# Performance work log

Measured on AMD Instinct MI355X. Metric: run time of the kernel, lower is better.

The kernel has to match this reference:

```python
import jax, jax.numpy as jnp
import numpy as np

# --- configuration (mirrors init_kwargs) ---
N_G = (256, 256, 128, 128)   # tem.hyper['n_g'] per-module sizes
N_ACTIONS = 4                 # tem action space
NUM_STATES = 4096
BATCH = 16384
G_TOTAL = sum(N_G)            # 768


def setup_inputs() -> dict:
    key = jax.random.key(0)
    ks = jax.random.split(key, 4 + len(N_G))
    inp = {
        "current_state_index": jax.random.randint(ks[0], (BATCH,), 0, NUM_STATES),
        "action_index": jax.random.randint(ks[1], (BATCH,), 0, N_ACTIONS),
        # xavier-ish init scale for embedding / classifier
        "emb": jax.random.normal(ks[2], (NUM_STATES, G_TOTAL), jnp.float32) * 0.02,
        "W_cls": jax.random.normal(ks[3], (NUM_STATES, G_TOTAL), jnp.float32) * 0.02,
        "b_cls": jnp.zeros((NUM_STATES,), jnp.float32),
    }
    # per-module bank of action-conditioned transition matrices D_a: [n_actions, n_g_f, n_g_f]
    for f, n in enumerate(N_G):
        inp[f"D{f}"] = jax.random.normal(ks[4 + f], (N_ACTIONS, n, n), jnp.float32) * (1.0 / np.sqrt(n))
    return inp


def _transition(g_f, D_f, onehot):
    # Routed action-conditioned transition (replaces the CPU per-action loop):
    # delta[b, j] = sum_i D_f[a_b, j, i] * g_f[b, i], dispatched via one-hot over actions.
    delta = jnp.einsum('aji,bi,ba->bj', D_f, g_f, onehot)
    # TEM generative clamp activation f_g_clamp
    return jnp.clip(g_f + delta, -1.0, 1.0)


def reference(current_state_index, action_index, emb, D0, D1, D2, D3, W_cls, b_cls):
    g_flat = emb[current_state_index]                                   # [B, G_TOTAL]
    onehot = jax.nn.one_hot(action_index, N_ACTIONS, dtype=g_flat.dtype)  # [B, A]
    # _split_g: slice flat grid code into TEM modules
    g_mods = jnp.split(g_flat, np.cumsum(np.array(N_G))[:-1].tolist(), axis=1)
    Ds = (D0, D1, D2, D3)
    g_next = [_transition(g_f, D_f, onehot) for g_f, D_f in zip(g_mods, Ds)]
    g_next_flat = jnp.concatenate(g_next, axis=1)                       # [B, G_TOTAL]
    logits = g_next_flat @ W_cls.T + b_cls                              # [B, NUM_STATES]
    return logits, g_next_flat
```

## Files before the change

### kernel.cpp

```cpp
#include <hip/hip_runtime.h>
#include <hip/hip_bf16.h>
#include <stdint.h>


typedef __attribute__((ext_vector_type(8))) short short8;
typedef __attribute__((ext_vector_type(4))) float floatx4;

__device__ __forceinline__ float bf2f(short s) {
    unsigned int u = ((unsigned int)(unsigned short)s) << 16;
    float f;
    __builtin_memcpy(&f, &u, 4);
    return f;
}
__device__ __forceinline__ short f2bf(float f) {
    unsigned int u;
    __builtin_memcpy(&u, &f, 4);
    u = (u + 0x7FFFu + ((u >> 16) & 1u)) >> 16;
    return (short)u;
}

#define GLLDS16(g, l)                                                                     \
    __builtin_amdgcn_global_load_lds((const __attribute__((address_space(1))) void*)(g),  \
                                     (__attribute__((address_space(3))) void*)(l), 16, 0, 0)

__global__ __launch_bounds__(256) void prep_kernel(
    const int* __restrict__ state, const float* __restrict__ emb,
    const float* __restrict__ W, const float* __restrict__ D0,
    const float* __restrict__ D1, const float* __restrict__ D2,
    const float* __restrict__ D3, short* __restrict__ A1,
    short* __restrict__ Wb, short* __restrict__ Db) {
    long e = (long)blockIdx.x * 256 + threadIdx.x;
    const float* src;
    short* dst;
    long di;
    if (e < 3145728L) {
        int b = (int)(e / 192);
        int cc = (int)(e % 192);
        int s = state[b];
        src = emb + (long)s * 768 + cc * 4;
        dst = A1; di = e;
    } else if (e < 3932160L) {
        long t = e - 3145728L;
        src = W + t * 4; dst = Wb; di = t;
    } else if (e < 3997696L) {
        long t = e - 3932160L;
        src = D0 + t * 4; dst = Db; di = t;
    } else if (e < 4063232L) {
        long t = e - 3997696L;
        src = D1 + t * 4; dst = Db + 262144; di = t;
    } else if (e < 4079616L) {
        long t = e - 4063232L;
        src = D2 + t * 4; dst = Db + 524288; di = t;
    } else {
        long t = e - 4079616L;
        src = D3 + t * 4; dst = Db + 589824; di = t;
    }
    float4 v = *(const float4*)src;
    union { ushort4 u4; short s4[4]; } o;
    o.s4[0] = f2bf(v.x); o.s4[1] = f2bf(v.y);
    o.s4[2] = f2bf(v.z); o.s4[3] = f2bf(v.w);
    *(ushort4*)(dst + di * 4) = o.u4;
}

__global__ __launch_bounds__(256) void trans_gemm_kernel(
    const short* __restrict__ A, const short* __restrict__ Bm,
    const int* __restrict__ act, float* __restrict__ gnext,
    short* __restrict__ A2, int n, int K) {
    __shared__ short Ash[128 * 64];
    __shared__ short Bsh[128 * 64];
    const int tid = threadIdx.x;
    const int lane = tid & 63;
    const int w = tid >> 6;
    const int wm = w & 1, wn = w >> 1;
    const int bn = blockIdx.x, bm = blockIdx.y;
    const long arow0 = (long)bm * 128;
    const long brow0 = (long)bn * 128;
    const int lrow = lane & 15;
    const int q = lane >> 4;

    floatx4 acc[4][4] = {};

    for (int k0 = 0; k0 < K; k0 += 64) {
        #pragma unroll
        for (int it = 0; it < 4; ++it) {
            int c = it * 256 + tid;
            int r = c >> 3, cc = c & 7;
            int gc = cc ^ (r & 7);
            GLLDS16(A + (arow0 + r) * 768 + k0 + gc * 8, &Ash[c * 8]);
            GLLDS16(Bm + (brow0 + r) * (long)n + k0 + gc * 8, &Bsh[c * 8]);
        }
        __syncthreads();
        #pragma unroll
        for (int kk = 0; kk < 2; ++kk) {
            short8 af[4], bv[4];
            #pragma unroll
            for (int mi = 0; mi < 4; ++mi) {
                int rr = wm * 64 + mi * 16 + lrow;
                int ch = (kk * 4 + q) ^ (rr & 7);
                af[mi] = *(const short8*)&Ash[rr * 64 + ch * 8];
            }
            #pragma unroll
            for (int ni = 0; ni < 4; ++ni) {
                int rr = wn * 64 + ni * 16 + lrow;
                int ch = (kk * 4 + q) ^ (rr & 7);
                bv[ni] = *(const short8*)&Bsh[rr * 64 + ch * 8];
            }
            #pragma unroll
            for (int mi = 0; mi < 4; ++mi)
                #pragma unroll
                for (int ni = 0; ni < 4; ++ni)
                    acc[mi][ni] = __builtin_amdgcn_mfma_f32_16x16x32_bf16(
                        af[mi], bv[ni], acc[mi][ni], 0, 0, 0);
        }
        __syncthreads();
    }

    const int tile_action = (bn * 128) / n;
    const int jb = bn * 128 - tile_action * n + wn * 64;
    const int rowbase = bm * 128 + wm * 64;
    #pragma unroll
    for (int mi = 0; mi < 4; ++mi) {
        #pragma unroll
        for (int r = 0; r < 4; ++r) {
            int row = rowbase + mi * 16 + q * 4 + r;
            if (act[row] == tile_action) {
                #pragma unroll
                for (int ni = 0; ni < 4; ++ni) {
                    int jl = jb + ni * 16 + lrow;
                    long idx = (long)row * 768 + jl;
                    float g = bf2f(A[idx]);
                    float v = g + acc[mi][ni][r];
                    v = fminf(1.0f, fmaxf(-1.0f, v));
                    gnext[idx] = v;
                    A2[idx] = f2bf(v);
                }
            }
        }
    }
}

__global__ __launch_bounds__(256) void cls_gemm_kernel(
    const short* __restrict__ A, const short* __restrict__ Bm,
    const float* __restrict__ bias, float* __restrict__ out) {
    __shared__ short Ash[128 * 64];
    __shared__ short Bsh[128 * 64];
    const int tid = threadIdx.x;
    const int lane = tid & 63;
    const int w = tid >> 6;
    const int wm = w & 1, wn = w >> 1;
    const int bn = blockIdx.x, bm = blockIdx.y;
    const long arow0 = (long)bm * 128;
    const long brow0 = (long)bn * 128;
    const int lrow = lane & 15;
    const int q = lane >> 4;

    floatx4 acc[4][4] = {};

    for (int k0 = 0; k0 < 768; k0 += 64) {
        #pragma unroll
        for (int it = 0; it < 4; ++it) {
            int c = it * 256 + tid;
            int r = c >> 3, cc = c & 7;
            int gc = cc ^ (r & 7);
            GLLDS16(A + (arow0 + r) * 768 + k0 + gc * 8, &Ash[c * 8]);
            GLLDS16(Bm + (brow0 + r) * 768 + k0 + gc * 8, &Bsh[c * 8]);
        }
        __syncthreads();
        #pragma unroll
        for (int kk = 0; kk < 2; ++kk) {
            short8 af[4], bv[4];
            #pragma unroll
            for (int mi = 0; mi < 4; ++mi) {
                int rr = wm * 64 + mi * 16 + lrow;
                int ch = (kk * 4 + q) ^ (rr & 7);
                af[mi] = *(const short8*)&Ash[rr * 64 + ch * 8];
            }
            #pragma unroll
            for (int ni = 0; ni < 4; ++ni) {
                int rr = wn * 64 + ni * 16 + lrow;
                int ch = (kk * 4 + q) ^ (rr & 7);
                bv[ni] = *(const short8*)&Bsh[rr * 64 + ch * 8];
            }
            #pragma unroll
            for (int mi = 0; mi < 4; ++mi)
                #pragma unroll
                for (int ni = 0; ni < 4; ++ni)
                    acc[mi][ni] = __builtin_amdgcn_mfma_f32_16x16x32_bf16(
                        af[mi], bv[ni], acc[mi][ni], 0, 0, 0);
        }
        __syncthreads();
    }

    const int rowbase = bm * 128 + wm * 64;
    const int colbase = bn * 128 + wn * 64;
    #pragma unroll
    for (int mi = 0; mi < 4; ++mi) {
        #pragma unroll
        for (int r = 0; r < 4; ++r) {
            int row = rowbase + mi * 16 + q * 4 + r;
            #pragma unroll
            for (int ni = 0; ni < 4; ++ni) {
                int col = colbase + ni * 16 + lrow;
                out[(long)row * 4096 + col] = acc[mi][ni][r] + bias[col];
            }
        }
    }
}

extern "C" void kernel_launch(void* const* d_in, const int* in_sizes, int n_in,
                              void* d_out, int out_size, void* d_ws, size_t ws_size,
                              hipStream_t stream) {
    const int* state  = (const int*)d_in[0];
    const int* act    = (const int*)d_in[1];
    const float* emb  = (const float*)d_in[2];
    const float* W    = (const float*)d_in[3];
    const float* bias = (const float*)d_in[4];
    const float* D0   = (const float*)d_in[5];
    const float* D1   = (const float*)d_in[6];
    const float* D2   = (const float*)d_in[7];
    const float* D3   = (const float*)d_in[8];

    float* logits = (float*)d_out;
    float* gnext  = logits + 67108864L;

    short* A1 = (short*)d_ws;
    short* A2 = A1 + 12582912L;
    short* Wb = A2 + 12582912L;
    short* Db = Wb + 3145728L;

    prep_kernel<<<16000, 256, 0, stream>>>(state, emb, W, D0, D1, D2, D3, A1, Wb, Db);

    trans_gemm_kernel<<<dim3(8, 128), 256, 0, stream>>>(A1, Db, act, gnext, A2, 256, 256);
    trans_gemm_kernel<<<dim3(8, 128), 256, 0, stream>>>(A1 + 256, Db + 262144, act,
                                                        gnext + 256, A2 + 256, 256, 256);
    trans_gemm_kernel<<<dim3(4, 128), 256, 0, stream>>>(A1 + 512, Db + 524288, act,
                                                        gnext + 512, A2 + 512, 128, 128);
    trans_gemm_kernel<<<dim3(4, 128), 256, 0, stream>>>(A1 + 640, Db + 589824, act,
                                                        gnext + 640, A2 + 640, 128, 128);

    cls_gemm_kernel<<<dim3(32, 128), 256, 0, stream>>>(A2, Wb, bias, logits);
}
```

Before: 541.0 us.

## Sort batch rows by action so transition GEMM computes only the matching action

```diff
diff --git a/kernel.cpp b/kernel.cpp
--- a/kernel.cpp
+++ b/kernel.cpp
@@ -23,12 +23,72 @@
     __builtin_amdgcn_global_load_lds((const __attribute__((address_space(1))) void*)(g),  \
                                      (__attribute__((address_space(3))) void*)(l), 16, 0, 0)
 
+#define ROWS_PAD 16896
+
+__global__ __launch_bounds__(1024) void setup_kernel(const int* __restrict__ act,
+                                                     int* __restrict__ meta,
+                                                     int* __restrict__ s2o) {
+    const int tid = threadIdx.x;
+    const int lane = tid & 63;
+    const int w = tid >> 6;
+    __shared__ int lc[16][4];
+    int c0 = 0, c1 = 0, c2 = 0, c3 = 0;
+    for (int i = tid; i < 16384; i += 1024) {
+        int a = act[i];
+        unsigned long long m0 = __ballot(a == 0);
+        unsigned long long m1 = __ballot(a == 1);
+        unsigned long long m2 = __ballot(a == 2);
+        unsigned long long m3 = __ballot(a == 3);
+        if (lane == 0) {
+            c0 += __popcll(m0); c1 += __popcll(m1);
+            c2 += __popcll(m2); c3 += __popcll(m3);
+        }
+    }
+    if (lane == 0) { lc[w][0] = c0; lc[w][1] = c1; lc[w][2] = c2; lc[w][3] = c3; }
+    for (int i = tid; i < ROWS_PAD; i += 1024) s2o[i] = -1;
+    __syncthreads();
+    if (tid == 0) {
+        int base = 0;
+        for (int k = 0; k < 4; ++k) {
+            int c = 0;
+            for (int ww = 0; ww < 16; ++ww) c += lc[ww][k];
+            meta[4 + k] = base;
+            meta[9 + k] = base;
+            base += (c + 127) & ~127;
+        }
+        meta[8] = base;
+    }
+}
+
+__global__ __launch_bounds__(256) void assign_kernel(const int* __restrict__ act,
+                                                     int* __restrict__ meta,
+                                                     int* __restrict__ slot_of,
+                                                     int* __restrict__ s2o) {
+    const int row = blockIdx.x * 256 + threadIdx.x;
+    const int lane = threadIdx.x & 63;
+    const int a = act[row];
+    const unsigned long long lt = (1ull << lane) - 1ull;
+    int* cursor = meta + 9;
+    int slot = 0;
+    #pragma unroll
+    for (int k = 0; k < 4; ++k) {
+        unsigned long long m = __ballot(a == k);
+        int c = __popcll(m);
+        int gb = 0;
+        if (lane == 0 && c) gb = atomicAdd(&cursor[k], c);
+        gb = __shfl(gb, 0);
+        if (a == k) slot = gb + __popcll(m & lt);
+    }
+    slot_of[row] = slot;
+    s2o[slot] = row;
+}
+
 __global__ __launch_bounds__(256) void prep_kernel(
-    const int* __restrict__ state, const float* __restrict__ emb,
-    const float* __restrict__ W, const float* __restrict__ D0,
-    const float* __restrict__ D1, const float* __restrict__ D2,
-    const float* __restrict__ D3, short* __restrict__ A1,
-    short* __restrict__ Wb, short* __restrict__ Db) {
+    const int* __restrict__ state, const int* __restrict__ slot_of,
+    const float* __restrict__ emb, const float* __restrict__ W,
+    const float* __restrict__ D0, const float* __restrict__ D1,
+    const float* __restrict__ D2, const float* __restrict__ D3,
+    short* __restrict__ A1, short* __restrict__ Wb, short* __restrict__ Db) {
     long e = (long)blockIdx.x * 256 + threadIdx.x;
     const float* src;
     short* dst;
@@ -37,8 +97,9 @@
         int b = (int)(e / 192);
         int cc = (int)(e % 192);
         int s = state[b];
+        int d = slot_of[b];
         src = emb + (long)s * 768 + cc * 4;
-        dst = A1; di = e;
+        dst = A1; di = (long)d * 192 + cc;
     } else if (e < 3932160L) {
         long t = e - 3145728L;
         src = W + t * 4; dst = Wb; di = t;
@@ -63,31 +124,48 @@
 }
 
 __global__ __launch_bounds__(256) void trans_gemm_kernel(
-    const short* __restrict__ A, const short* __restrict__ Bm,
-    const int* __restrict__ act, float* __restrict__ gnext,
-    short* __restrict__ A2, int n, int K) {
+    const short* __restrict__ A, const short* __restrict__ Db,
+    const int* __restrict__ meta, const int* __restrict__ s2o,
+    float* __restrict__ gnext, short* __restrict__ A2) {
     __shared__ short Ash[128 * 64];
     __shared__ short Bsh[128 * 64];
+    const int bx = blockIdx.x, bm = blockIdx.y;
+    int n, bn, coloff;
+    long Doff;
+    if (bx < 4) {
+        n = 256; bn = bx & 1;
+        int f = bx >> 1;
+        coloff = f * 256; Doff = (long)f * 262144;
+    } else {
+        n = 128; bn = 0;
+        int f = bx - 4;
+        coloff = 512 + f * 128; Doff = 524288 + (long)f * 65536;
+    }
+    const int rowbase = bm * 128;
+    const int sb4 = meta[8];
+    if (rowbase >= sb4) return;
+    const int a = (rowbase >= meta[5]) + (rowbase >= meta[6]) + (rowbase >= meta[7]);
+    const short* Bm = Db + Doff + (long)a * n * n;
+
     const int tid = threadIdx.x;
     const int lane = tid & 63;
     const int w = tid >> 6;
     const int wm = w & 1, wn = w >> 1;
-    const int bn = blockIdx.x, bm = blockIdx.y;
-    const long arow0 = (long)bm * 128;
+    const long arow0 = (long)rowbase;
     const long brow0 = (long)bn * 128;
     const int lrow = lane & 15;
     const int q = lane >> 4;
 
     floatx4 acc[4][4] = {};
 
-    for (int k0 = 0; k0 < K; k0 += 64) {
+    for (int k0 = 0; k0 < n; k0 += 64) {
         #pragma unroll
         for (int it = 0; it < 4; ++it) {
             int c = it * 256 + tid;
             int r = c >> 3, cc = c & 7;
             int gc = cc ^ (r & 7);
-            GLLDS16(A + (arow0 + r) * 768 + k0 + gc * 8, &Ash[c * 8]);
-            GLLDS16(Bm + (brow0 + r) * (long)n + k0 + gc * 8, &Bsh[c * 8]);
+            GLLDS16(A + (arow0 + r) * 768 + coloff + k0 + gc * 8, &Ash[c * 8]);
+            GLLDS16(Bm + (brow0 + r) * n + k0 + gc * 8, &Bsh[c * 8]);
         }
         __syncthreads();
         #pragma unroll
@@ -115,24 +193,24 @@
         __syncthreads();
     }
 
-    const int tile_action = (bn * 128) / n;
-    const int jb = bn * 128 - tile_action * n + wn * 64;
-    const int rowbase = bm * 128 + wm * 64;
+    const int jb = bn * 128 + wn * 64;
+    const int rowb2 = rowbase + wm * 64;
     #pragma unroll
     for (int mi = 0; mi < 4; ++mi) {
         #pragma unroll
         for (int r = 0; r < 4; ++r) {
-            int row = rowbase + mi * 16 + q * 4 + r;
-            if (act[row] == tile_action) {
+            int srow = rowb2 + mi * 16 + q * 4 + r;
+            int orig = s2o[srow];
+            if (orig >= 0) {
                 #pragma unroll
                 for (int ni = 0; ni < 4; ++ni) {
                     int jl = jb + ni * 16 + lrow;
-                    long idx = (long)row * 768 + jl;
-                    float g = bf2f(A[idx]);
+                    long sidx = (long)srow * 768 + coloff + jl;
+                    float g = bf2f(A[sidx]);
                     float v = g + acc[mi][ni][r];
                     v = fminf(1.0f, fmaxf(-1.0f, v));
-                    gnext[idx] = v;
-                    A2[idx] = f2bf(v);
+                    gnext[(long)orig * 768 + coloff + jl] = v;
+                    A2[sidx] = f2bf(v);
                 }
             }
         }
@@ -141,15 +219,18 @@
 
 __global__ __launch_bounds__(256) void cls_gemm_kernel(
     const short* __restrict__ A, const short* __restrict__ Bm,
-    const float* __restrict__ bias, float* __restrict__ out) {
+    const float* __restrict__ bias, const int* __restrict__ meta,
+    const int* __restrict__ s2o, float* __restrict__ out) {
     __shared__ short Ash[128 * 64];
     __shared__ short Bsh[128 * 64];
+    const int bn = blockIdx.x, bm = blockIdx.y;
+    const int rowbase = bm * 128;
+    if (rowbase >= meta[8]) return;
     const int tid = threadIdx.x;
     const int lane = tid & 63;
     const int w = tid >> 6;
     const int wm = w & 1, wn = w >> 1;
-    const int bn = blockIdx.x, bm = blockIdx.y;
-    const long arow0 = (long)bm * 128;
+    const long arow0 = (long)rowbase;
     const long brow0 = (long)bn * 128;
     const int lrow = lane & 15;
     const int q = lane >> 4;
@@ -191,17 +272,20 @@
         __syncthreads();
     }
 
-    const int rowbase = bm * 128 + wm * 64;
+    const int rowb2 = rowbase + wm * 64;
     const int colbase = bn * 128 + wn * 64;
     #pragma unroll
     for (int mi = 0; mi < 4; ++mi) {
         #pragma unroll
         for (int r = 0; r < 4; ++r) {
-            int row = rowbase + mi * 16 + q * 4 + r;
-            #pragma unroll
-            for (int ni = 0; ni < 4; ++ni) {
-                int col = colbase + ni * 16 + lrow;
-                out[(long)row * 4096 + col] = acc[mi][ni][r] + bias[col];
+            int srow = rowb2 + mi * 16 + q * 4 + r;
+            int orig = s2o[srow];
+            if (orig >= 0) {
+                #pragma unroll
+                for (int ni = 0; ni < 4; ++ni) {
+                    int col = colbase + ni * 16 + lrow;
+                    out[(long)orig * 4096 + col] = acc[mi][ni][r] + bias[col];
+                }
             }
         }
     }
@@ -224,19 +308,17 @@
     float* gnext  = logits + 67108864L;
 
     short* A1 = (short*)d_ws;
-    short* A2 = A1 + 12582912L;
-    short* Wb = A2 + 12582912L;
+    short* A2 = A1 + 12976128L;
+    short* Wb = A2 + 12976128L;
     short* Db = Wb + 3145728L;
-
-    prep_kernel<<<16000, 256, 0, stream>>>(state, emb, W, D0, D1, D2, D3, A1, Wb, Db);
-
-    trans_gemm_kernel<<<dim3(8, 128), 256, 0, stream>>>(A1, Db, act, gnext, A2, 256, 256);
-    trans_gemm_kernel<<<dim3(8, 128), 256, 0, stream>>>(A1 + 256, Db + 262144, act,
-                                                        gnext + 256, A2 + 256, 256, 256);
-    trans_gemm_kernel<<<dim3(4, 128), 256, 0, stream>>>(A1 + 512, Db + 524288, act,
-                                                        gnext + 512, A2 + 512, 128, 128);
-    trans_gemm_kernel<<<dim3(4, 128), 256, 0, stream>>>(A1 + 640, Db + 589824, act,
-                                                        gnext + 640, A2 + 640, 128, 128);
-
-    cls_gemm_kernel<<<dim3(32, 128), 256, 0, stream>>>(A2, Wb, bias, logits);
-}
+    int* meta    = (int*)(Db + 655360);
+    int* slot_of = meta + 16;
+    int* s2o     = slot_of + 16384;
+
+    setup_kernel<<<1, 1024, 0, stream>>>(act, meta, s2o);
+    assign_kernel<<<64, 256, 0, stream>>>(act, meta, slot_of, s2o);
+    prep_kernel<<<16000, 256, 0, stream>>>(state, slot_of, emb, W, D0, D1, D2, D3,
+                                           A1, Wb, Db);
+    trans_gemm_kernel<<<dim3(6, 132), 256, 0, stream>>>(A1, Db, meta, s2o, gnext, A2);
+    cls_gemm_kernel<<<dim3(32, 132), 256, 0, stream>>>(A2, Wb, bias, meta, s2o, logits);
+}
```

New measurement: 565.9 us. 1.05x slower.
